# Kernel tuning notes

Measured on AMD Instinct MI355X. Metric: run time of the kernel, lower is better.

Reference implementation:

```python
import jax, jax.numpy as jnp
import numpy as np

IN_DIM = 1024
BS, NCROPS = 32, 1024


def setup_inputs() -> dict:
    key = jax.random.key(0)
    ks = jax.random.split(key, 7)
    s = 1.0 / np.sqrt(IN_DIM)
    return {
        "x": jax.random.normal(ks[0], (BS, NCROPS, IN_DIM), jnp.float32),
        "Wq": jax.random.uniform(ks[1], (IN_DIM,), jnp.float32, -s, s),
        "bq": jax.random.uniform(ks[2], (1,), jnp.float32, -s, s),
        "Wk": jax.random.uniform(ks[3], (IN_DIM,), jnp.float32, -s, s),
        "bk": jax.random.uniform(ks[4], (1,), jnp.float32, -s, s),
        "Wv": jax.random.uniform(ks[5], (IN_DIM, IN_DIM), jnp.float32, -s, s),
        "bv": jax.random.uniform(ks[6], (IN_DIM,), jnp.float32, -s, s),
    }


def reference(x, Wq, bq, Wk, bk, Wv, bv):
    # x: (bs, n, d). 1x1 Conv1d over permuted x == per-position linear maps.
    bs, n, d = x.shape
    q = jnp.einsum("bnd,d->bn", x, Wq) + bq  # (bs, n)   query_conv -> 1 channel
    k = jnp.einsum("bnd,d->bn", x, Wk) + bk  # (bs, n)   key_conv   -> 1 channel
    energy = q[:, :, None] * k[:, None, :]    # (bs, n, n) rank-1 outer product (bmm of (n,1)@(1,n))
    attention = jax.nn.softmax(energy, axis=-1)
    v = jnp.einsum("od,bnd->bon", Wv, x) + bv[None, :, None]  # (bs, d, n) value_conv
    out = jnp.einsum("bdn,bnm->bdm", v, attention)            # (bs, d, n)
    # Faithful to torch .view: raw reshape of (bs, d, n) -> (bs, n, d), NOT a transpose.
    out = out.reshape(bs, n, d)
    return (out, attention)
```

## Files before the change

kernel.cpp:

```cpp
#include <hip/hip_runtime.h>
#include <hip/hip_bf16.h>

#define BS  32
#define N   1024
#define DIM 1024

typedef unsigned short u16;
typedef unsigned int   u32;

typedef __attribute__((ext_vector_type(8))) __bf16 bf16x8;
typedef __attribute__((ext_vector_type(4))) float  f32x4;

__device__ __forceinline__ u16 f2bf(float f) {
    u32 u = __builtin_bit_cast(u32, f);
    u = (u + 0x7FFF + ((u >> 16) & 1)) >> 16;
    return (u16)u;
}

__device__ __forceinline__ void async16(const u16* g, u16* l) {
    __builtin_amdgcn_global_load_lds(
        (const __attribute__((address_space(1))) u32*)g,
        (__attribute__((address_space(3))) u32*)l,
        16, 0, 0);
}

__global__ void convert_qk(const float* __restrict__ x,
                           const float* __restrict__ Wq, const float* __restrict__ bq,
                           const float* __restrict__ Wk, const float* __restrict__ bk,
                           const float* __restrict__ Wv,
                           u16* __restrict__ xb, u16* __restrict__ Wvb,
                           float* __restrict__ qv, float* __restrict__ kv)
{
    int gw   = (blockIdx.x * 256 + threadIdx.x) >> 6;
    int lane = threadIdx.x & 63;
    bool isX = gw < BS * N;
    const float* src = isX ? (x + (size_t)gw * DIM) : (Wv + (size_t)(gw - BS * N) * DIM);
    u16*         dst = isX ? (xb + (size_t)gw * DIM) : (Wvb + (size_t)(gw - BS * N) * DIM);
    float qd = 0.f, kd = 0.f;
    #pragma unroll
    for (int i = 0; i < 4; ++i) {
        int e = i * 256 + lane * 4;
        float4 xv = *(const float4*)&src[e];
        uint2 p;
        p.x = (u32)f2bf(xv.x) | ((u32)f2bf(xv.y) << 16);
        p.y = (u32)f2bf(xv.z) | ((u32)f2bf(xv.w) << 16);
        *(uint2*)&dst[e] = p;
        if (isX) {
            float4 wq = *(const float4*)&Wq[e];
            float4 wk = *(const float4*)&Wk[e];
            qd += xv.x * wq.x + xv.y * wq.y + xv.z * wq.z + xv.w * wq.w;
            kd += xv.x * wk.x + xv.y * wk.y + xv.z * wk.z + xv.w * wk.w;
        }
    }
    if (isX) {
        #pragma unroll
        for (int off = 32; off; off >>= 1) {
            qd += __shfl_xor(qd, off);
            kd += __shfl_xor(kd, off);
        }
        if (lane == 0) { qv[gw] = qd + bq[0]; kv[gw] = kd + bk[0]; }
    }
}

__global__ void att_writer(const float* __restrict__ qv, const float* __restrict__ kvg,
                           float* __restrict__ att, float2* __restrict__ qzg)
{
    int blk = blockIdx.x;
    int b   = blk >> 6;
    int r0  = (blk & 63) * 16;
    __shared__ float ks[1024];
    int tid = threadIdx.x;
    #pragma unroll
    for (int i = 0; i < 4; ++i) ks[i * 256 + tid] = kvg[b * N + i * 256 + tid];
    int row = tid >> 4;
    int c16 = tid & 15;
    float qrow = qv[b * N + r0 + row];
    __syncthreads();
    float z = 0.f;
    #pragma unroll 4
    for (int s = 0; s < 16; ++s) {
        const float4 kk = *(const float4*)&ks[(c16 + s * 16) * 4];
        z += __expf(qrow * kk.x) + __expf(qrow * kk.y)
           + __expf(qrow * kk.z) + __expf(qrow * kk.w);
    }
    z += __shfl_xor(z, 1); z += __shfl_xor(z, 2);
    z += __shfl_xor(z, 4); z += __shfl_xor(z, 8);
    float invZ = 1.0f / z;
    if (c16 == 0) qzg[b * N + r0 + row] = make_float2(qrow, invZ);
    float* ab = att + (size_t)b * N * N + (size_t)(r0 + row) * N;
    #pragma unroll 4
    for (int s = 0; s < 16; ++s) {
        int c0 = (c16 + s * 16) * 4;
        const float4 kk = *(const float4*)&ks[c0];
        float4 o;
        o.x = __expf(qrow * kk.x) * invZ;
        o.y = __expf(qrow * kk.y) * invZ;
        o.z = __expf(qrow * kk.z) * invZ;
        o.w = __expf(qrow * kk.w) * invZ;
        *(float4*)&ab[c0] = o;
    }
}

__global__ __launch_bounds__(256) void gemm_bt(
    const u16* __restrict__ A,
    const u16* __restrict__ B, size_t bBatch,
    u16* __restrict__ C, size_t cBatch,
    const float* __restrict__ bias)
{
    const int K = 1024, LD = 1024;
    int blk  = blockIdx.x;
    int rest = blk >> 3;
    int b    = (blk & 7) * 4 + (rest >> 6);
    int t    = rest & 63;
    int m0  = (t >> 3) * 128, n0 = (t & 7) * 128;
    const u16* Ab = A;
    const u16* Bb = B + bBatch * (size_t)b;
    __shared__ u16 lA[128 * 32];
    __shared__ u16 lB[128 * 32];
    int w = threadIdx.x >> 6, lane = threadIdx.x & 63;
    int wr = (w >> 1) * 64, wc = (w & 1) * 64;
    int rowl = lane >> 2;
    int col8 = (lane & 3) * 8;
    int frow = lane & 15, fk = (lane >> 4) * 8;
    f32x4 acc[4][4] = {};

    for (int k0 = 0; k0 < K; k0 += 32) {
        #pragma unroll
        for (int s = 0; s < 2; ++s) {
            int rr = (s * 4 + w) * 16;
            async16(Ab + (size_t)(m0 + rr + rowl) * LD + k0 + col8, &lA[rr * 32]);
            async16(Bb + (size_t)(n0 + rr + rowl) * LD + k0 + col8, &lB[rr * 32]);
        }
        __syncthreads();
        bf16x8 af[4], bfr[4];
        #pragma unroll
        for (int i = 0; i < 4; ++i)
            af[i] = *(const bf16x8*)&lA[(wr + i * 16 + frow) * 32 + fk];
        #pragma unroll
        for (int j = 0; j < 4; ++j)
            bfr[j] = *(const bf16x8*)&lB[(wc + j * 16 + frow) * 32 + fk];
        #pragma unroll
        for (int i = 0; i < 4; ++i)
            #pragma unroll
            for (int j = 0; j < 4; ++j)
                acc[i][j] = __builtin_amdgcn_mfma_f32_16x16x32_bf16(af[i], bfr[j], acc[i][j], 0, 0, 0);
        __syncthreads();
    }

    int r4 = (lane >> 4) * 4, cc = lane & 15;
    u16* Cb = C + cBatch * (size_t)b;
    #pragma unroll
    for (int i = 0; i < 4; ++i)
        #pragma unroll
        for (int j = 0; j < 4; ++j)
            #pragma unroll
            for (int rg = 0; rg < 4; ++rg) {
                int row = m0 + wr + i * 16 + r4 + rg;
                int col = n0 + wc + j * 16 + cc;
                Cb[(size_t)row * LD + col] = f2bf(acc[i][j][rg] + bias[row]);
            }
}

__global__ __launch_bounds__(256) void gemm2_fused(
    const u16* __restrict__ A,
    const float2* __restrict__ qzg,
    const float* __restrict__ kvg,
    float* __restrict__ C)
{
    const int K = 1024, LD = 1024;
    int blk  = blockIdx.x;
    int rest = blk >> 3;
    int b    = (blk & 7) * 4 + (rest >> 6);
    int t    = rest & 63;
    int m0  = (t >> 3) * 128, n0 = (t & 7) * 128;
    const u16* Ab = A + (size_t)b * K * LD;
    __shared__ u16   lA[128 * 32];
    __shared__ float2 qz[1024];
    int tid = threadIdx.x;
    int w = tid >> 6, lane = tid & 63;
    int wr = (w >> 1) * 64, wc = (w & 1) * 64;
    int rowl = lane >> 2;
    int col8 = (lane & 3) * 8;
    int frow = lane & 15, fk = (lane >> 4) * 8;

    const float2* qzb = qzg + (size_t)b * N;
    #pragma unroll
    for (int i = 0; i < 4; ++i) qz[i * 256 + tid] = qzb[i * 256 + tid];
    float kk[4];
    #pragma unroll
    for (int j = 0; j < 4; ++j) kk[j] = kvg[(size_t)b * N + n0 + wc + j * 16 + frow];
    f32x4 acc[4][4] = {};
    __syncthreads();

    for (int k0 = 0; k0 < K; k0 += 32) {
        #pragma unroll
        for (int s = 0; s < 2; ++s) {
            int rr = (s * 4 + w) * 16;
            async16(Ab + (size_t)(m0 + rr + rowl) * LD + k0 + col8, &lA[rr * 32]);
        }
        const float4* qsrc = (const float4*)&qz[k0 + fk];
        float4 qp[4];
        #pragma unroll
        for (int u = 0; u < 4; ++u) qp[u] = qsrc[u];
        bf16x8 bfr[4];
        #pragma unroll
        for (int j = 0; j < 4; ++j) {
            union { u32 u[4]; bf16x8 v; } pk;
            #pragma unroll
            for (int u = 0; u < 4; ++u) {
                float e0 = __expf(qp[u].x * kk[j]) * qp[u].y;
                float e1 = __expf(qp[u].z * kk[j]) * qp[u].w;
                pk.u[u] = (u32)f2bf(e0) | ((u32)f2bf(e1) << 16);
            }
            bfr[j] = pk.v;
        }
        __syncthreads();
        bf16x8 af[4];
        #pragma unroll
        for (int i = 0; i < 4; ++i)
            af[i] = *(const bf16x8*)&lA[(wr + i * 16 + frow) * 32 + fk];
        #pragma unroll
        for (int i = 0; i < 4; ++i)
            #pragma unroll
            for (int j = 0; j < 4; ++j)
                acc[i][j] = __builtin_amdgcn_mfma_f32_16x16x32_bf16(af[i], bfr[j], acc[i][j], 0, 0, 0);
        __syncthreads();
    }

    int r4 = (lane >> 4) * 4, cc = lane & 15;
    float* Cb = C + (size_t)b * K * LD;
    #pragma unroll
    for (int i = 0; i < 4; ++i)
        #pragma unroll
        for (int j = 0; j < 4; ++j)
            #pragma unroll
            for (int rg = 0; rg < 4; ++rg) {
                int row = m0 + wr + i * 16 + r4 + rg;
                int col = n0 + wc + j * 16 + cc;
                Cb[(size_t)row * LD + col] = acc[i][j][rg];
            }
}

extern "C" void kernel_launch(void* const* d_in, const int* in_sizes, int n_in,
                              void* d_out, int out_size, void* d_ws, size_t ws_size,
                              hipStream_t stream)
{
    const float* x  = (const float*)d_in[0];
    const float* Wq = (const float*)d_in[1];
    const float* bq = (const float*)d_in[2];
    const float* Wk = (const float*)d_in[3];
    const float* bk = (const float*)d_in[4];
    const float* Wv = (const float*)d_in[5];
    const float* bv = (const float*)d_in[6];

    float* out = (float*)d_out;
    float* att = out + (size_t)BS * N * N;

    char* ws = (char*)d_ws;
    u16*  xb   = (u16*)ws;
    u16*  vb   = xb + (size_t)BS * N * DIM;
    u16*  Wvb  = vb + (size_t)BS * N * DIM;
    float* qv  = (float*)(Wvb + (size_t)DIM * DIM);
    float* kv  = qv + BS * N;
    float2* qzg = (float2*)(kv + BS * N);

    convert_qk<<<(BS * N + DIM) / 4, 256, 0, stream>>>(x, Wq, bq, Wk, bk, Wv, xb, Wvb, qv, kv);
    att_writer<<<BS * 64, 256, 0, stream>>>(qv, kv, att, qzg);
    gemm_bt<<<BS * 64, 256, 0, stream>>>(Wvb, xb, (size_t)N * DIM, vb, (size_t)N * DIM, bv);
    gemm2_fused<<<BS * 64, 256, 0, stream>>>(vb, qzg, kv, out);
}
```

Measured before the change: 603.3 us.

## Materialize transposed bf16 attention and use plain GEMM instead of fused exp

The attention softmax is no longer recomputed inside the second GEMM. A new tiled kernel writes the fp32 attention output and also a transposed bf16 copy to workspace. The second GEMM then loads both operands from memory via async LDS loads. This removes the per-tile exp recomputation from the GEMM inner loop, at the cost of an extra 64MB bf16 write and read plus an extra kernel launch.

```diff
diff --git a/kernel.cpp b/kernel.cpp
--- a/kernel.cpp
+++ b/kernel.cpp
@@ -62,8 +62,8 @@
     }
 }
 
-__global__ void att_writer(const float* __restrict__ qv, const float* __restrict__ kvg,
-                           float* __restrict__ att, float2* __restrict__ qzg)
+__global__ void qz_writer(const float* __restrict__ qv, const float* __restrict__ kvg,
+                          float2* __restrict__ qzg)
 {
     int blk = blockIdx.x;
     int b   = blk >> 6;
@@ -85,19 +85,50 @@
     }
     z += __shfl_xor(z, 1); z += __shfl_xor(z, 2);
     z += __shfl_xor(z, 4); z += __shfl_xor(z, 8);
-    float invZ = 1.0f / z;
-    if (c16 == 0) qzg[b * N + r0 + row] = make_float2(qrow, invZ);
-    float* ab = att + (size_t)b * N * N + (size_t)(r0 + row) * N;
-    #pragma unroll 4
-    for (int s = 0; s < 16; ++s) {
-        int c0 = (c16 + s * 16) * 4;
-        const float4 kk = *(const float4*)&ks[c0];
-        float4 o;
-        o.x = __expf(qrow * kk.x) * invZ;
-        o.y = __expf(qrow * kk.y) * invZ;
-        o.z = __expf(qrow * kk.z) * invZ;
-        o.w = __expf(qrow * kk.w) * invZ;
-        *(float4*)&ab[c0] = o;
+    if (c16 == 0) qzg[b * N + r0 + row] = make_float2(qrow, 1.0f / z);
+}
+
+__global__ void att_tiles(const float2* __restrict__ qzg, const float* __restrict__ kvg,
+                          float* __restrict__ att, u16* __restrict__ attT)
+{
+    int blk  = blockIdx.x;
+    int b    = blk >> 8;
+    int rest = blk & 255;
+    int r0 = (rest >> 4) * 64;
+    int c0 = (rest & 15) * 64;
+    int tid = threadIdx.x;
+    int tx = tid & 15, ty = tid >> 4;
+
+    float q[4], iz[4];
+    #pragma unroll
+    for (int i = 0; i < 4; ++i) {
+        float2 p = qzg[(size_t)b * N + r0 + tx * 4 + i];
+        q[i] = p.x; iz[i] = p.y;
+    }
+    float kvj[4];
+    #pragma unroll
+    for (int j = 0; j < 4; ++j) kvj[j] = kvg[(size_t)b * N + c0 + ty * 4 + j];
+
+    float e[4][4];
+    #pragma unroll
+    for (int i = 0; i < 4; ++i)
+        #pragma unroll
+        for (int j = 0; j < 4; ++j)
+            e[i][j] = __expf(q[i] * kvj[j]) * iz[i];
+
+    float* ab = att + (size_t)b * N * N;
+    #pragma unroll
+    for (int i = 0; i < 4; ++i) {
+        float4 o = make_float4(e[i][0], e[i][1], e[i][2], e[i][3]);
+        *(float4*)&ab[(size_t)(r0 + tx * 4 + i) * N + c0 + ty * 4] = o;
+    }
+    u16* tb = attT + (size_t)b * N * N;
+    #pragma unroll
+    for (int j = 0; j < 4; ++j) {
+        uint2 p;
+        p.x = (u32)f2bf(e[0][j]) | ((u32)f2bf(e[1][j]) << 16);
+        p.y = (u32)f2bf(e[2][j]) | ((u32)f2bf(e[3][j]) << 16);
+        *(uint2*)&tb[(size_t)(c0 + ty * 4 + j) * N + r0 + tx * 4] = p;
     }
 }
 
@@ -161,11 +192,10 @@
             }
 }
 
-__global__ __launch_bounds__(256) void gemm2_fused(
-    const u16* __restrict__ A,
-    const float2* __restrict__ qzg,
-    const float* __restrict__ kvg,
-    float* __restrict__ C)
+__global__ __launch_bounds__(256) void gemm2_bt(
+    const u16* __restrict__ A, size_t aBatch,
+    const u16* __restrict__ B, size_t bBatch,
+    float* __restrict__ C, size_t cBatch)
 {
     const int K = 1024, LD = 1024;
     int blk  = blockIdx.x;
@@ -173,52 +203,32 @@
     int b    = (blk & 7) * 4 + (rest >> 6);
     int t    = rest & 63;
     int m0  = (t >> 3) * 128, n0 = (t & 7) * 128;
-    const u16* Ab = A + (size_t)b * K * LD;
-    __shared__ u16   lA[128 * 32];
-    __shared__ float2 qz[1024];
-    int tid = threadIdx.x;
-    int w = tid >> 6, lane = tid & 63;
+    const u16* Ab = A + aBatch * (size_t)b;
+    const u16* Bb = B + bBatch * (size_t)b;
+    __shared__ u16 lA[128 * 32];
+    __shared__ u16 lB[128 * 32];
+    int w = threadIdx.x >> 6, lane = threadIdx.x & 63;
     int wr = (w >> 1) * 64, wc = (w & 1) * 64;
     int rowl = lane >> 2;
     int col8 = (lane & 3) * 8;
     int frow = lane & 15, fk = (lane >> 4) * 8;
-
-    const float2* qzb = qzg + (size_t)b * N;
-    #pragma unroll
-    for (int i = 0; i < 4; ++i) qz[i * 256 + tid] = qzb[i * 256 + tid];
-    float kk[4];
-    #pragma unroll
-    for (int j = 0; j < 4; ++j) kk[j] = kvg[(size_t)b * N + n0 + wc + j * 16 + frow];
     f32x4 acc[4][4] = {};
-    __syncthreads();
 
     for (int k0 = 0; k0 < K; k0 += 32) {
         #pragma unroll
         for (int s = 0; s < 2; ++s) {
             int rr = (s * 4 + w) * 16;
             async16(Ab + (size_t)(m0 + rr + rowl) * LD + k0 + col8, &lA[rr * 32]);
-        }
-        const float4* qsrc = (const float4*)&qz[k0 + fk];
-        float4 qp[4];
-        #pragma unroll
-        for (int u = 0; u < 4; ++u) qp[u] = qsrc[u];
-        bf16x8 bfr[4];
-        #pragma unroll
-        for (int j = 0; j < 4; ++j) {
-            union { u32 u[4]; bf16x8 v; } pk;
-            #pragma unroll
-            for (int u = 0; u < 4; ++u) {
-                float e0 = __expf(qp[u].x * kk[j]) * qp[u].y;
-                float e1 = __expf(qp[u].z * kk[j]) * qp[u].w;
-                pk.u[u] = (u32)f2bf(e0) | ((u32)f2bf(e1) << 16);
-            }
-            bfr[j] = pk.v;
-        }
-        __syncthreads();
-        bf16x8 af[4];
+            async16(Bb + (size_t)(n0 + rr + rowl) * LD + k0 + col8, &lB[rr * 32]);
+        }
+        __syncthreads();
+        bf16x8 af[4], bfr[4];
         #pragma unroll
         for (int i = 0; i < 4; ++i)
             af[i] = *(const bf16x8*)&lA[(wr + i * 16 + frow) * 32 + fk];
+        #pragma unroll
+        for (int j = 0; j < 4; ++j)
+            bfr[j] = *(const bf16x8*)&lB[(wc + j * 16 + frow) * 32 + fk];
         #pragma unroll
         for (int i = 0; i < 4; ++i)
             #pragma unroll
@@ -228,7 +238,7 @@
     }
 
     int r4 = (lane >> 4) * 4, cc = lane & 15;
-    float* Cb = C + (size_t)b * K * LD;
+    float* Cb = C + cBatch * (size_t)b;
     #pragma unroll
     for (int i = 0; i < 4; ++i)
         #pragma unroll
@@ -263,9 +273,11 @@
     float* qv  = (float*)(Wvb + (size_t)DIM * DIM);
     float* kv  = qv + BS * N;
     float2* qzg = (float2*)(kv + BS * N);
+    u16*  attT = (u16*)(qzg + BS * N);
 
     convert_qk<<<(BS * N + DIM) / 4, 256, 0, stream>>>(x, Wq, bq, Wk, bk, Wv, xb, Wvb, qv, kv);
-    att_writer<<<BS * 64, 256, 0, stream>>>(qv, kv, att, qzg);
+    qz_writer<<<BS * 64, 256, 0, stream>>>(qv, kv, qzg);
     gemm_bt<<<BS * 64, 256, 0, stream>>>(Wvb, xb, (size_t)N * DIM, vb, (size_t)N * DIM, bv);
-    gemm2_fused<<<BS * 64, 256, 0, stream>>>(vb, qzg, kv, out);
-}
+    att_tiles<<<BS * 256, 256, 0, stream>>>(qzg, kv, att, attT);
+    gemm2_bt<<<BS * 64, 256, 0, stream>>>(vb, (size_t)N * DIM, attT, (size_t)N * N, out, (size_t)N * DIM);
+}
```

New measurement: 609.1 us. No clear change (+1.0%).
